# Performance work log

Hardware: AMD Instinct MI355X
Metric: run time of the kernel (lower is better)

The kernel has to match this reference:

```python
import jax, jax.numpy as jnp
import numpy as np
from jax import lax

D = 1024          # channel / embedding dim
K = 2048          # codebook size
BN_EPS = 1e-5


def conv1d(x, w, b, stride):
    # x: [N, C, L], w: [O, I, k]
    y = lax.conv_general_dilated(x, w, window_strides=(stride,), padding='VALID',
                                 dimension_numbers=('NCH', 'OIH', 'NCH'))
    return y + b[None, :, None]


def batchnorm1d(x, gamma, beta):
    # training-mode BN: batch statistics over (N, L) per channel, biased variance
    mean = jnp.mean(x, axis=(0, 2), keepdims=True)
    var = jnp.var(x, axis=(0, 2), keepdims=True)
    return (x - mean) * lax.rsqrt(var + BN_EPS) * gamma[None, :, None] + beta[None, :, None]


def setup_inputs() -> dict:
    key = jax.random.key(0)
    ks = jax.random.split(key, 8)
    x = jax.random.normal(ks[0], (32, D, 1024), dtype=jnp.float32)
    conv1_w = jax.random.normal(ks[1], (D, D, 4), dtype=jnp.float32) * 0.02
    conv1_b = jnp.zeros((D,), dtype=jnp.float32)
    bn1_g = jnp.ones((D,), dtype=jnp.float32)
    bn1_b = jnp.zeros((D,), dtype=jnp.float32)
    conv2_w = jax.random.normal(ks[2], (D, D, 1), dtype=jnp.float32) * 0.02
    conv2_b = jnp.zeros((D,), dtype=jnp.float32)
    bn2_g = jnp.ones((D,), dtype=jnp.float32)
    bn2_b = jnp.zeros((D,), dtype=jnp.float32)
    codebook = jax.random.normal(ks[3], (K, D), dtype=jnp.float32)
    return {'x': x, 'conv1_w': conv1_w, 'conv1_b': conv1_b,
            'bn1_g': bn1_g, 'bn1_b': bn1_b,
            'conv2_w': conv2_w, 'conv2_b': conv2_b,
            'bn2_g': bn2_g, 'bn2_b': bn2_b,
            'codebook': codebook}


def encoder(x, conv1_w, conv1_b, bn1_g, bn1_b, conv2_w, conv2_b, bn2_g, bn2_b):
    h = conv1d(x, conv1_w, conv1_b, stride=2)           # [B, D, L']
    # ResidualWrapper(BN -> ReLU -> Conv1x1)
    r = batchnorm1d(h, bn1_g, bn1_b)
    r = jax.nn.relu(r)
    r = conv1d(r, conv2_w, conv2_b, stride=1)
    h = h + r
    h = batchnorm1d(h, bn2_g, bn2_b)
    return h


def vq(h, codebook):
    # axis=1 -> move channel axis last: [B, L', D]
    z = jnp.moveaxis(h, 1, -1)
    # squared Euclidean distances via ||z||^2 - 2 z.e + ||e||^2  (cdist+argmin)
    z2 = jnp.sum(z * z, axis=-1, keepdims=True)                  # [B, L', 1]
    e2 = jnp.sum(codebook * codebook, axis=-1)                   # [K]
    ze = jnp.einsum('bld,kd->blk', z, codebook)                  # [B, L', K]
    dist2 = z2 - 2.0 * ze + e2[None, None, :]
    ids = jnp.argmin(dist2, axis=-1)                             # [B, L'] int
    q = codebook[ids]                                            # [B, L', D]
    sg = lax.stop_gradient
    commitment = jnp.mean((z - sg(q)) ** 2)
    codebook_loss = jnp.mean((sg(z) - q) ** 2)
    # straight-through estimator
    q_st = z + sg(q - z)
    q_st = jnp.moveaxis(q_st, -1, 1)                             # back to [B, D, L']
    return q_st, ids, commitment, codebook_loss


def reference(x, conv1_w, conv1_b, bn1_g, bn1_b, conv2_w, conv2_b, bn2_g, bn2_b, codebook):
    h = encoder(x, conv1_w, conv1_b, bn1_g, bn1_b, conv2_w, conv2_b, bn2_g, bn2_b)
    q_st, ids, commitment, codebook_loss = vq(h, codebook)
    return q_st, ids, commitment, codebook_loss
```

## Files before the change

### kernel.cpp

```cpp
#include <hip/hip_runtime.h>
#include <hip/hip_bf16.h>
#include <cstdint>

#define DD 1024
#define LIN 1024
#define LP 511
#define LPAD 512
#define NBATCH 32
#define KCB 2048
#define BN_EPS 1e-5f

#define OUT_IDS 16744448u
#define OUT_LOSS 16760800u

#define WS_H1 0
#define WS_UNI 16777216
#define WS_XH  (WS_UNI)
#define WS_XL  (WS_UNI + 16777728)
#define WS_WTH (WS_UNI + 33555456)
#define WS_WTL (WS_UNI + 35652608)
#define WS_T2  (WS_UNI)
#define WS_RH  (WS_UNI + 16777216)
#define WS_RL  (WS_UNI + 25165824)
#define WS_ZH  WS_RH
#define WS_ZL  WS_RL
#define WS_W2H (WS_UNI + 33554432)
#define WS_W2L (WS_UNI + 34078720)
#define WS_CBH (WS_UNI + 34603008)
#define WS_CBL (WS_UNI + 35651584)
#define WS_AUX (WS_UNI + 37749760)
#define WS_A1 (WS_AUX + 0)
#define WS_B1 (WS_AUX + 1024)
#define WS_A2 (WS_AUX + 2048)
#define WS_B2 (WS_AUX + 3072)
#define WS_E2 (WS_AUX + 4096)
#define WS_SLOTS (WS_AUX + 6144)
#define WS_LOSS (WS_AUX + 6144 + 32704)

typedef __attribute__((ext_vector_type(8))) short bf16x8;
typedef __attribute__((ext_vector_type(4))) float f32x4;
typedef __attribute__((ext_vector_type(16))) float f32x16;
typedef __attribute__((ext_vector_type(4))) unsigned short ushort4v;

__device__ __forceinline__ void async_cp16(const void* gsrc, void* ldst) {
  __builtin_amdgcn_global_load_lds(
      (const __attribute__((address_space(1))) unsigned int*)gsrc,
      (__attribute__((address_space(3))) unsigned int*)ldst, 16, 0, 0);
}

__device__ __forceinline__ void bf16split(float v, unsigned short& hi, unsigned short& lo) {
  __hip_bfloat16 h = __float2bfloat16(v);
  float hf = __bfloat162float(h);
  __hip_bfloat16 l = __float2bfloat16(v - hf);
  hi = *(unsigned short*)&h;
  lo = *(unsigned short*)&l;
}

__device__ inline float blockReduce256(float v, float* sb) {
#pragma unroll
  for (int off = 32; off > 0; off >>= 1) v += __shfl_down(v, off);
  __syncthreads();
  if ((threadIdx.x & 63) == 0) sb[threadIdx.x >> 6] = v;
  __syncthreads();
  return sb[0] + sb[1] + sb[2] + sb[3];
}

#define VMCNT(n) asm volatile("s_waitcnt vmcnt(" #n ")" ::: "memory")

template <typename SF>
__device__ __forceinline__ void stage_slot(const SF& sf, int c, int slot,
                                           unsigned short* smbase, int wid,
                                           int lane) {
  int plane, r0;
  if (slot < 4) {
    plane = 2 + (slot >> 1);
    r0 = ((slot & 1) << 7) + (wid << 4);
  } else {
    plane = wid & 1;
    r0 = (((wid >> 1) & 1) << 7) + ((slot - 4) << 5) + ((wid >> 2) << 4);
  }
  const unsigned short* g = sf(c, plane) + (size_t)(r0 + (lane >> 2)) * 1024 +
                            (((lane & 3) ^ ((lane >> 3) & 3)) << 3);
  unsigned short* d = smbase + plane * 8192 + r0 * 32;
  async_cp16(g, d);
}

template <typename SF>
__device__ __forceinline__ void mfma256_core32(const SF& sf, unsigned short* sm,
                                               int nkc, f32x16 (&acc)[4][2]) {
  const int tid = threadIdx.x;
  const int wid = tid >> 6, lane = tid & 63;
  const int wm = wid >> 2, wn = wid & 3;
  const int lrow = lane & 31;
  const int khalf = lane >> 5;
  const int sig = (lane >> 1) & 3;
  const int arowb = (wm << 7) + lrow;
  const int browb = (wn << 6) + lrow;

#pragma unroll
  for (int s = 0; s < 8; ++s) stage_slot(sf, 0, s, sm, wid, lane);

  bf16x8 fbh[2][2], fbl[2][2];
  for (int c = 0; c < nkc; ++c) {
    unsigned short* buf = sm + ((c & 1) << 15);
    unsigned short* nbuf = sm + (((c + 1) & 1) << 15);
    const unsigned short* As = buf;
    const unsigned short* Als = buf + 8192;
    const unsigned short* Bs = buf + 16384;
    const unsigned short* Bls = buf + 24576;
    const bool pre = (c + 1 < nkc);
#pragma unroll
    for (int q = 0; q < 2; ++q) {
      if (q == 0) {
        VMCNT(2);
      } else if (pre) {
        VMCNT(4);
      } else {
        VMCNT(0);
      }
      __builtin_amdgcn_s_barrier();
      asm volatile("" ::: "memory");
      __builtin_amdgcn_sched_barrier(0);
      if (q == 0) {
#pragma unroll
        for (int nt = 0; nt < 2; ++nt) {
          const int r = browb + nt * 32;
#pragma unroll
          for (int kh = 0; kh < 2; ++kh) {
            const int off = r * 32 + ((((kh << 1) + khalf) ^ sig) << 3);
            fbh[kh][nt] = *(const bf16x8*)(Bs + off);
            fbl[kh][nt] = *(const bf16x8*)(Bls + off);
          }
        }
      }
      bf16x8 fah[2][2], fal[2][2];
#pragma unroll
      for (int mi = 0; mi < 2; ++mi) {
        const int r = arowb + ((q << 1) + mi) * 32;
#pragma unroll
        for (int kh = 0; kh < 2; ++kh) {
          const int off = r * 32 + ((((kh << 1) + khalf) ^ sig) << 3);
          fah[mi][kh] = *(const bf16x8*)(As + off);
          fal[mi][kh] = *(const bf16x8*)(Als + off);
        }
      }
      if (pre) {
#pragma unroll
        for (int s = 0; s < 4; ++s)
          stage_slot(sf, c + 1, (q << 2) + s, nbuf, wid, lane);
      }
      __builtin_amdgcn_s_setprio(1);
#pragma unroll
      for (int kh = 0; kh < 2; ++kh) {
#pragma unroll
        for (int t = 0; t < 3; ++t) {
#pragma unroll
          for (int mi = 0; mi < 2; ++mi) {
#pragma unroll
            for (int nt = 0; nt < 2; ++nt) {
              const bf16x8 af = (t == 2) ? fal[mi][kh] : fah[mi][kh];
              const bf16x8 bb = (t == 1) ? fbl[kh][nt] : fbh[kh][nt];
              acc[(q << 1) + mi][nt] = __builtin_amdgcn_mfma_f32_32x32x16_bf16(
                  af, bb, acc[(q << 1) + mi][nt], 0, 0, 0);
            }
          }
        }
      }
      __builtin_amdgcn_s_setprio(0);
    }
  }
}

__global__ __launch_bounds__(256) void split_w1_kernel(
    const float* __restrict__ w, unsigned short* __restrict__ wth,
    unsigned short* __restrict__ wtl) {
  int idx = blockIdx.x * 256 + threadIdx.x;
  int o = idx >> 10, i = idx & 1023;
  float4 v = *(const float4*)&w[(size_t)idx * 4];
  float vv[4] = {v.x, v.y, v.z, v.w};
#pragma unroll
  for (int t = 0; t < 4; ++t) {
    unsigned short hi, lo;
    bf16split(vv[t], hi, lo);
    size_t off = (((size_t)(t << 10) + o) << 10) + i;
    wth[off] = hi;
    wtl[off] = lo;
  }
}

__global__ __launch_bounds__(256) void split_rows_kernel(
    const float* __restrict__ src, unsigned short* __restrict__ dsth,
    unsigned short* __restrict__ dstl) {
  size_t base = ((size_t)blockIdx.x * 256 + threadIdx.x) * 4;
  float4 v = *(const float4*)&src[base];
  float vv[4] = {v.x, v.y, v.z, v.w};
  ushort4v h, l;
#pragma unroll
  for (int j = 0; j < 4; ++j) {
    unsigned short hi, lo;
    bf16split(vv[j], hi, lo);
    h[j] = hi;
    l[j] = lo;
  }
  *(ushort4v*)&dsth[base] = h;
  *(ushort4v*)&dstl[base] = l;
}

__global__ __launch_bounds__(256) void split_x_kernel(
    const float* __restrict__ x, unsigned short* __restrict__ xh,
    unsigned short* __restrict__ xl) {
  __shared__ float lsT[128 * 65];
  const int l0 = blockIdx.x * 128;
  const int i0 = blockIdx.y * 64;
  const int nB = blockIdx.z;
  const int tid = threadIdx.x;
#pragma unroll
  for (int p = 0; p < 8; ++p) {
    int flat = p * 256 + tid;
    int row = flat >> 5, col4 = (flat & 31) * 4;
    float4 v = *(const float4*)&x[((size_t)nB * DD + i0 + row) * LIN + l0 + col4];
    lsT[(col4 + 0) * 65 + row] = v.x;
    lsT[(col4 + 1) * 65 + row] = v.y;
    lsT[(col4 + 2) * 65 + row] = v.z;
    lsT[(col4 + 3) * 65 + row] = v.w;
  }
  __syncthreads();
  const int lo2 = (l0 >> 1);
#pragma unroll
  for (int p = 0; p < 16; ++p) {
    int cp = p * 4 + (tid >> 6);
    int il = tid & 63;
    float vE = lsT[(2 * cp) * 65 + il];
    float vO = lsT[(2 * cp + 1) * 65 + il];
    unsigned short hE, lE, hO, lO;
    bf16split(vE, hE, lE);
    bf16split(vO, hO, lO);
    size_t dE = (((size_t)(0 * 32 + nB) * 512) + lo2 + cp) * 1024 + i0 + il;
    size_t dO = (((size_t)(1 * 32 + nB) * 512) + lo2 + cp) * 1024 + i0 + il;
    xh[dE] = hE; xl[dE] = lE;
    xh[dO] = hO; xl[dO] = lO;
  }
}

__global__ __launch_bounds__(256) void trans_affine_split_kernel(
    const float* __restrict__ src, const float* __restrict__ a,
    const float* __restrict__ b, unsigned short* __restrict__ dsth,
    unsigned short* __restrict__ dstl, int do_relu) {
  __shared__ float lsT[128 * 65];
  const int l0 = blockIdx.x * 128;
  const int i0 = blockIdx.y * 64;
  const int nB = blockIdx.z;
  const int tid = threadIdx.x;
#pragma unroll
  for (int p = 0; p < 8; ++p) {
    int flat = p * 256 + tid;
    int row = flat >> 5, col4 = (flat & 31) * 4;
    float4 v = *(const float4*)&src[((size_t)nB * DD + i0 + row) * LPAD + l0 + col4];
    lsT[(col4 + 0) * 65 + row] = v.x;
    lsT[(col4 + 1) * 65 + row] = v.y;
    lsT[(col4 + 2) * 65 + row] = v.z;
    lsT[(col4 + 3) * 65 + row] = v.w;
  }
  __syncthreads();
  const int il = tid & 63;
  const float ac = a[i0 + il], bc = b[i0 + il];
#pragma unroll
  for (int p = 0; p < 32; ++p) {
    int cp = p * 4 + (tid >> 6);
    float v = fmaf(ac, lsT[cp * 65 + il], bc);
    if (do_relu) v = fmaxf(v, 0.f);
    unsigned short hi, lo;
    bf16split(v, hi, lo);
    size_t d = (((size_t)nB * 512) + l0 + cp) * 1024 + i0 + il;
    dsth[d] = hi;
    dstl[d] = lo;
  }
}

__global__ __launch_bounds__(512, 2) void conv1_mfma_kernel(
    const unsigned short* __restrict__ wth, const unsigned short* __restrict__ wtl,
    const unsigned short* __restrict__ xh, const unsigned short* __restrict__ xl,
    const float* __restrict__ bias, float* __restrict__ h1) {
  extern __shared__ unsigned short sm[];
  const int tid = threadIdx.x;
  const int wid = tid >> 6, lane = tid & 63;
  const int lin = blockIdx.x;
  const int lb = (lin & 1) * 256;
  const int nB = ((lin >> 1) & 3) | ((lin >> 5) << 2);
  const int ob = ((lin >> 3) & 3) * 256;

  f32x16 acc[4][2];
#pragma unroll
  for (int a = 0; a < 4; ++a)
#pragma unroll
    for (int b = 0; b < 2; ++b)
#pragma unroll
      for (int e = 0; e < 16; ++e) acc[a][b][e] = 0.f;

  auto sf = [&](int c, int plane) -> const unsigned short* {
    int t = c >> 5, kc = c & 31;
    if (plane == 0) return wth + ((((size_t)t << 10) + ob) << 10) + kc * 32;
    if (plane == 1) return wtl + ((((size_t)t << 10) + ob) << 10) + kc * 32;
    const unsigned short* xp = (plane == 2) ? xh : xl;
    return xp + ((((size_t)((t & 1) * 32 + nB) * 512) + lb + (t >> 1)) << 10) + kc * 32;
  };
  mfma256_core32(sf, sm, 128, acc);

  const int wm = wid >> 2, wn = wid & 3;
#pragma unroll
  for (int mt = 0; mt < 4; ++mt) {
#pragma unroll
    for (int nt = 0; nt < 2; ++nt) {
      const int l = lb + (wn << 6) + nt * 32 + (lane & 31);
      if (l < LP) {
#pragma unroll
        for (int rq = 0; rq < 4; ++rq) {
          const int o0 = ob + (wm << 7) + mt * 32 + rq * 8 + ((lane >> 5) << 2);
#pragma unroll
          for (int rg = 0; rg < 4; ++rg)
            h1[((size_t)(nB << 10) + o0 + rg) * LPAD + l] =
                acc[mt][nt][rq * 4 + rg] + bias[o0 + rg];
        }
      }
    }
  }
}

__global__ __launch_bounds__(512, 2) void conv2_mfma_kernel(
    const unsigned short* __restrict__ w2h, const unsigned short* __restrict__ w2l,
    const unsigned short* __restrict__ rh, const unsigned short* __restrict__ rl,
    const float* __restrict__ b2c, const float* __restrict__ h1,
    float* __restrict__ t2) {
  extern __shared__ unsigned short sm[];
  const int tid = threadIdx.x;
  const int wid = tid >> 6, lane = tid & 63;
  const int lin = blockIdx.x;
  const int lb = (lin & 1) * 256;
  const int nB = ((lin >> 1) & 3) | ((lin >> 5) << 2);
  const int ob = ((lin >> 3) & 3) * 256;

  f32x16 acc[4][2];
#pragma unroll
  for (int a = 0; a < 4; ++a)
#pragma unroll
    for (int b = 0; b < 2; ++b)
#pragma unroll
      for (int e = 0; e < 16; ++e) acc[a][b][e] = 0.f;

  auto sf = [&](int c, int plane) -> const unsigned short* {
    if (plane == 0) return w2h + ((size_t)ob << 10) + (size_t)c * 32;
    if (plane == 1) return w2l + ((size_t)ob << 10) + (size_t)c * 32;
    const unsigned short* rp = (plane == 2) ? rh : rl;
    return rp + (((size_t)nB * 512 + lb) << 10) + (size_t)c * 32;
  };
  mfma256_core32(sf, sm, 32, acc);

  const int wm = wid >> 2, wn = wid & 3;
#pragma unroll
  for (int mt = 0; mt < 4; ++mt) {
#pragma unroll
    for (int nt = 0; nt < 2; ++nt) {
      const int l = lb + (wn << 6) + nt * 32 + (lane & 31);
      if (l < LP) {
#pragma unroll
        for (int rq = 0; rq < 4; ++rq) {
          const int o0 = ob + (wm << 7) + mt * 32 + rq * 8 + ((lane >> 5) << 2);
#pragma unroll
          for (int rg = 0; rg < 4; ++rg) {
            size_t off = ((size_t)(nB << 10) + o0 + rg) * LPAD + l;
            t2[off] = h1[off] + acc[mt][nt][rq * 4 + rg] + b2c[o0 + rg];
          }
        }
      }
    }
  }
}

__global__ __launch_bounds__(512, 2) void dist_mfma_kernel(
    const unsigned short* __restrict__ cbh, const unsigned short* __restrict__ cbl,
    const unsigned short* __restrict__ zh, const unsigned short* __restrict__ zl,
    const float* __restrict__ e2, unsigned long long* __restrict__ slots) {
  extern __shared__ unsigned short sm[];
  unsigned long long* best = (unsigned long long*)(sm + 65536);
  const int tid = threadIdx.x;
  const int wid = tid >> 6, lane = tid & 63;
  const int lb = blockIdx.x * 256, kb = blockIdx.y * 256, nB = blockIdx.z;

  if (tid < 256) best[tid] = ~0ULL;

  f32x16 acc[4][2];
#pragma unroll
  for (int a = 0; a < 4; ++a)
#pragma unroll
    for (int b = 0; b < 2; ++b)
#pragma unroll
      for (int e = 0; e < 16; ++e) acc[a][b][e] = 0.f;

  auto sf = [&](int c, int plane) -> const unsigned short* {
    if (plane == 0) return cbh + ((size_t)kb << 10) + (size_t)c * 32;
    if (plane == 1) return cbl + ((size_t)kb << 10) + (size_t)c * 32;
    const unsigned short* zp = (plane == 2) ? zh : zl;
    return zp + (((size_t)nB * 512 + lb) << 10) + (size_t)c * 32;
  };
  mfma256_core32(sf, sm, 32, acc);

  const int wm = wid >> 2, wn = wid & 3;
#pragma unroll
  for (int nt = 0; nt < 2; ++nt) {
    const int col = (wn << 6) + nt * 32 + (lane & 31);
    float dmin = 3.4e38f;
    int kmin = 0;
#pragma unroll
    for (int mt = 0; mt < 4; ++mt) {
#pragma unroll
      for (int rq = 0; rq < 4; ++rq) {
        const int kbase = kb + (wm << 7) + mt * 32 + rq * 8 + ((lane >> 5) << 2);
#pragma unroll
        for (int rg = 0; rg < 4; ++rg) {
          float dist = fmaf(-2.f, acc[mt][nt][rq * 4 + rg], e2[kbase + rg]);
          if (dist < dmin) { dmin = dist; kmin = kbase + rg; }
        }
      }
    }
    unsigned long long pk =
        ((unsigned long long)__float_as_uint(dmin) << 32) | (unsigned)kmin;
    atomicMin(&best[col], pk);
  }
  __syncthreads();
  if (tid < 256) {
    int l = lb + tid;
    if (l < LP) atomicMin(&slots[(size_t)nB * LP + l], best[tid]);
  }
}

__global__ __launch_bounds__(256) void bn_stats_kernel(
    const float* __restrict__ src, const float* __restrict__ gamma,
    const float* __restrict__ beta, float* __restrict__ a_out,
    float* __restrict__ b_out) {
  __shared__ float sb[4];
  const int c = blockIdx.x;
  const float* p = src + (size_t)c * LPAD;
  float s1 = 0.f, s2 = 0.f;
  for (int idx = threadIdx.x; idx < NBATCH * LP; idx += 256) {
    int nn = idx / LP;
    int l = idx - nn * LP;
    float v = p[(size_t)nn * DD * LPAD + l];
    s1 += v;
    s2 = fmaf(v, v, s2);
  }
  s1 = blockReduce256(s1, sb);
  s2 = blockReduce256(s2, sb);
  if (threadIdx.x == 0) {
    const float inv = 1.f / (float)(NBATCH * LP);
    float m = s1 * inv;
    float var = fmaf(-m, m, s2 * inv);
    float a = gamma[c] * rsqrtf(var + BN_EPS);
    a_out[c] = a;
    b_out[c] = fmaf(-m, a, beta[c]);
  }
}

__global__ __launch_bounds__(256) void e2_kernel(const float* __restrict__ cb,
                                                 float* __restrict__ e2) {
  __shared__ float sb[4];
  const int k = blockIdx.x;
  float s = 0.f;
  for (int d = threadIdx.x; d < DD; d += 256) {
    float v = cb[(size_t)k * DD + d];
    s = fmaf(v, v, s);
  }
  s = blockReduce256(s, sb);
  if (threadIdx.x == 0) e2[k] = s;
}

__global__ __launch_bounds__(256) void gather_kernel(
    const float* __restrict__ t2, const float* __restrict__ cb,
    const float* __restrict__ a2, const float* __restrict__ b2,
    const unsigned long long* __restrict__ slots, float* __restrict__ out,
    float* __restrict__ loss_acc) {
  __shared__ int ks[64];
  __shared__ float sb[4];
  const int l0 = blockIdx.x * 64;
  const int n = blockIdx.y;
  const int tid = threadIdx.x, tx = tid & 63, ty = tid >> 6;
  if (tid < 64) {
    int l = l0 + tid;
    int k = 0;
    if (l < LP) {
      k = (int)(unsigned)(slots[(size_t)n * LP + l] & 0xffffffffULL);
      out[OUT_IDS + (size_t)n * LP + l] = (float)k;
    }
    ks[tid] = k;
  }
  __syncthreads();
  const int l = l0 + tx;
  const bool valid = (l < LP);
  const int k = ks[tx];
  const float* cbk = cb + (size_t)k * DD;
  const float* tn = t2 + (size_t)n * DD * LPAD;
  float* qo = out + (size_t)n * DD * LP;
  float lsum = 0.f;
  for (int d0 = 0; d0 < DD; d0 += 4) {
    const int d = d0 + ty;
    float q = cbk[d];
    if (valid) {
      float z = fmaf(a2[d], tn[(size_t)d * LPAD + l], b2[d]);
      qo[(size_t)d * LP + l] = q;
      float e = z - q;
      lsum = fmaf(e, e, lsum);
    }
  }
  lsum = blockReduce256(lsum, sb);
  if (tid == 0) atomicAdd(loss_acc, lsum);
}

__global__ void finalize_kernel(const float* __restrict__ loss_acc,
                                float* __restrict__ out) {
  if (threadIdx.x == 0) {
    float m = loss_acc[0] * (1.f / 16744448.f);
    out[OUT_LOSS] = m;
    out[OUT_LOSS + 1] = m;
  }
}

extern "C" void kernel_launch(void* const* d_in, const int* in_sizes, int n_in,
                              void* d_out, int out_size, void* d_ws,
                              size_t ws_size, hipStream_t stream) {
  const float* x = (const float*)d_in[0];
  const float* w1 = (const float*)d_in[1];
  const float* b1c = (const float*)d_in[2];
  const float* g1 = (const float*)d_in[3];
  const float* be1 = (const float*)d_in[4];
  const float* w2 = (const float*)d_in[5];
  const float* b2c = (const float*)d_in[6];
  const float* g2 = (const float*)d_in[7];
  const float* be2 = (const float*)d_in[8];
  const float* cb = (const float*)d_in[9];
  float* out = (float*)d_out;
  float* ws = (float*)d_ws;

  float* h1 = ws + WS_H1;
  float* t2 = ws + WS_T2;
  unsigned short* xh = (unsigned short*)(ws + WS_XH);
  unsigned short* xl = (unsigned short*)(ws + WS_XL);
  unsigned short* wth = (unsigned short*)(ws + WS_WTH);
  unsigned short* wtl = (unsigned short*)(ws + WS_WTL);
  unsigned short* rh = (unsigned short*)(ws + WS_RH);
  unsigned short* rl = (unsigned short*)(ws + WS_RL);
  unsigned short* zh = (unsigned short*)(ws + WS_ZH);
  unsigned short* zl = (unsigned short*)(ws + WS_ZL);
  unsigned short* w2h = (unsigned short*)(ws + WS_W2H);
  unsigned short* w2l = (unsigned short*)(ws + WS_W2L);
  unsigned short* cbh = (unsigned short*)(ws + WS_CBH);
  unsigned short* cbl = (unsigned short*)(ws + WS_CBL);
  float* a1 = ws + WS_A1;
  float* bb1 = ws + WS_B1;
  float* a2 = ws + WS_A2;
  float* bb2 = ws + WS_B2;
  float* e2 = ws + WS_E2;
  unsigned long long* slots = (unsigned long long*)(ws + WS_SLOTS);
  float* loss = ws + WS_LOSS;

  static int attr_done = 0;
  if (!attr_done) {
    (void)hipFuncSetAttribute(reinterpret_cast<const void*>(conv1_mfma_kernel),
                              hipFuncAttributeMaxDynamicSharedMemorySize, 135168);
    (void)hipFuncSetAttribute(reinterpret_cast<const void*>(conv2_mfma_kernel),
                              hipFuncAttributeMaxDynamicSharedMemorySize, 135168);
    (void)hipFuncSetAttribute(reinterpret_cast<const void*>(dist_mfma_kernel),
                              hipFuncAttributeMaxDynamicSharedMemorySize, 135168);
    attr_done = 1;
  }

  (void)hipMemsetAsync(slots, 0xFF,
                       (size_t)NBATCH * LP * sizeof(unsigned long long), stream);
  (void)hipMemsetAsync(loss, 0, sizeof(float), stream);

  split_w1_kernel<<<4096, 256, 0, stream>>>(w1, wth, wtl);
  split_x_kernel<<<dim3(8, 16, NBATCH), 256, 0, stream>>>(x, xh, xl);
  conv1_mfma_kernel<<<256, 512, 131072, stream>>>(wth, wtl, xh, xl, b1c, h1);
  bn_stats_kernel<<<DD, 256, 0, stream>>>(h1, g1, be1, a1, bb1);
  split_rows_kernel<<<1024, 256, 0, stream>>>(w2, w2h, w2l);
  split_rows_kernel<<<2048, 256, 0, stream>>>(cb, cbh, cbl);
  e2_kernel<<<KCB, 256, 0, stream>>>(cb, e2);
  trans_affine_split_kernel<<<dim3(4, 16, NBATCH), 256, 0, stream>>>(
      h1, a1, bb1, rh, rl, 1);
  conv2_mfma_kernel<<<256, 512, 131072, stream>>>(w2h, w2l, rh, rl, b2c, h1, t2);
  bn_stats_kernel<<<DD, 256, 0, stream>>>(t2, g2, be2, a2, bb2);
  trans_affine_split_kernel<<<dim3(4, 16, NBATCH), 256, 0, stream>>>(
      t2, a2, bb2, zh, zl, 0);
  dist_mfma_kernel<<<dim3(2, 8, NBATCH), 512, 133120, stream>>>(cbh, cbl, zh,
                                                                zl, e2, slots);
  gather_kernel<<<dim3(8, NBATCH), 256, 0, stream>>>(t2, cb, a2, bb2, slots, out, loss);
  finalize_kernel<<<1, 64, 0, stream>>>(loss, out);
}
```

Measured before the change: 1.025 ms.

## Software-pipeline MFMA GEMM core with register prefetch of next-chunk LDS fragments

Rewrites the bf16x3 MFMA main loop as a manually unrolled two-chunk pipeline. Fragments for the next k-chunk are read from LDS into registers while the current chunk's MFMAs run, and global-to-LDS staging is issued two chunks ahead in split halves. The aim is to hide LDS read latency and barrier stalls behind matrix instructions. The cost is higher register pressure and more complex wait-count logic, and the loop now assumes an even chunk count of at least 2.

```diff
diff --git a/kernel.cpp b/kernel.cpp
--- a/kernel.cpp
+++ b/kernel.cpp
@@ -85,6 +85,101 @@
   async_cp16(g, d);
 }
 
+template <int PH>
+__device__ __forceinline__ void mfma_half(f32x16 (&acc)[4][2],
+                                          const bf16x8 (&ah)[2],
+                                          const bf16x8 (&al)[2],
+                                          const bf16x8 (&bh)[2],
+                                          const bf16x8 (&bl)[2]) {
+#pragma unroll
+  for (int t = 0; t < 3; ++t)
+#pragma unroll
+    for (int mi = 0; mi < 2; ++mi)
+#pragma unroll
+      for (int nt = 0; nt < 2; ++nt) {
+        const bf16x8 af = (t == 2) ? al[mi] : ah[mi];
+        const bf16x8 bb = (t == 1) ? bl[nt] : bh[nt];
+        acc[PH * 2 + mi][nt] = __builtin_amdgcn_mfma_f32_32x32x16_bf16(
+            af, bb, acc[PH * 2 + mi][nt], 0, 0, 0);
+      }
+}
+
+#define FRAG(BASE, ROW, SIDX) \
+  (*(const bf16x8*)((BASE) + (ROW) * 32 + (((SIDX) ^ sig) << 3)))
+
+#define CHUNK_BODY(CIDX, PP, NX1, NX2)                                        \
+  {                                                                           \
+    const int c__ = (CIDX);                                                   \
+    unsigned short* bufc = sm + ((PP) << 15);                                 \
+    unsigned short* bufn = sm + (((PP) ^ 1) << 15);                           \
+    const unsigned short* As = bufc;                                          \
+    const unsigned short* Als = bufc + 8192;                                  \
+    const unsigned short* Bs = bufc + 16384;                                  \
+    const unsigned short* Bls = bufc + 24576;                                 \
+    const unsigned short* Asn = bufn;                                         \
+    const unsigned short* Alsn = bufn + 8192;                                 \
+    const unsigned short* Bsn = bufn + 16384;                                 \
+    const unsigned short* Blsn = bufn + 24576;                                \
+                                                            \
+    if (NX1) { VMCNT(4); } else { VMCNT(0); }                                 \
+    __builtin_amdgcn_s_barrier();                                             \
+    __builtin_amdgcn_sched_barrier(0);                                        \
+    _Pragma("unroll") for (int mi = 0; mi < 2; ++mi) {                        \
+      const int r = arowb + mi * 32;                                          \
+      a0h[1][mi] = FRAG(As, r, 2 + khalf);                                    \
+      a0l[1][mi] = FRAG(Als, r, 2 + khalf);                                   \
+    }                                                                         \
+    _Pragma("unroll") for (int nt = 0; nt < 2; ++nt) {                        \
+      const int r = browb + nt * 32;                                          \
+      bh1[nt] = FRAG(Bs, r, 2 + khalf);                                       \
+      bl1[nt] = FRAG(Bls, r, 2 + khalf);                                      \
+    }                                                                         \
+    _Pragma("unroll") for (int mi = 0; mi < 2; ++mi) {                        \
+      const int r = arowb + (2 + mi) * 32;                                    \
+      a1h[0][mi] = FRAG(As, r, khalf);                                        \
+      a1l[0][mi] = FRAG(Als, r, khalf);                                       \
+    }                                                                         \
+    if (NX1) {                                                                \
+      _Pragma("unroll") for (int s = 4; s < 8; ++s)                           \
+          stage_slot(sf, c__ + 1, s, bufn, wid, lane);                        \
+    }                                                                         \
+    __builtin_amdgcn_sched_barrier(0);                                        \
+    __builtin_amdgcn_s_setprio(1);                                            \
+    mfma_half<0>(acc, a0h[0], a0l[0], bh0[PP], bl0[PP]);                      \
+    mfma_half<0>(acc, a0h[1], a0l[1], bh1, bl1);                              \
+    __builtin_amdgcn_s_setprio(0);                                            \
+                                                            \
+    if (NX1) { VMCNT(2); } else { VMCNT(0); }                                 \
+    __builtin_amdgcn_s_barrier();                                             \
+    __builtin_amdgcn_sched_barrier(0);                                        \
+    _Pragma("unroll") for (int mi = 0; mi < 2; ++mi) {                        \
+      const int r = arowb + (2 + mi) * 32;                                    \
+      a1h[1][mi] = FRAG(As, r, 2 + khalf);                                    \
+      a1l[1][mi] = FRAG(Als, r, 2 + khalf);                                   \
+    }                                                                         \
+    if (NX1) {                                                                \
+      _Pragma("unroll") for (int nt = 0; nt < 2; ++nt) {                      \
+        const int r = browb + nt * 32;                                        \
+        bh0[(PP) ^ 1][nt] = FRAG(Bsn, r, khalf);                              \
+        bl0[(PP) ^ 1][nt] = FRAG(Blsn, r, khalf);                             \
+      }                                                                       \
+      _Pragma("unroll") for (int mi = 0; mi < 2; ++mi) {                      \
+        const int r = arowb + mi * 32;                                        \
+        a0h[0][mi] = FRAG(Asn, r, khalf);                                     \
+        a0l[0][mi] = FRAG(Alsn, r, khalf);                                    \
+      }                                                                       \
+    }                                                                         \
+    if (NX2) {                                                                \
+      _Pragma("unroll") for (int s = 0; s < 4; ++s)                           \
+          stage_slot(sf, c__ + 2, s, bufc, wid, lane);                        \
+    }                                                                         \
+    __builtin_amdgcn_sched_barrier(0);                                        \
+    __builtin_amdgcn_s_setprio(1);                                            \
+    mfma_half<1>(acc, a1h[0], a1l[0], bh0[PP], bl0[PP]);                      \
+    mfma_half<1>(acc, a1h[1], a1l[1], bh1, bl1);                              \
+    __builtin_amdgcn_s_setprio(0);                                            \
+  }
+
 template <typename SF>
 __device__ __forceinline__ void mfma256_core32(const SF& sf, unsigned short* sm,
                                                int nkc, f32x16 (&acc)[4][2]) {
@@ -97,78 +192,43 @@
   const int arowb = (wm << 7) + lrow;
   const int browb = (wn << 6) + lrow;
 
+  bf16x8 a0h[2][2], a0l[2][2];
+  bf16x8 a1h[2][2], a1l[2][2];
+  bf16x8 bh0[2][2], bl0[2][2];
+  bf16x8 bh1[2], bl1[2];
+
 #pragma unroll
   for (int s = 0; s < 8; ++s) stage_slot(sf, 0, s, sm, wid, lane);
-
-  bf16x8 fbh[2][2], fbl[2][2];
-  for (int c = 0; c < nkc; ++c) {
-    unsigned short* buf = sm + ((c & 1) << 15);
-    unsigned short* nbuf = sm + (((c + 1) & 1) << 15);
-    const unsigned short* As = buf;
-    const unsigned short* Als = buf + 8192;
-    const unsigned short* Bs = buf + 16384;
-    const unsigned short* Bls = buf + 24576;
-    const bool pre = (c + 1 < nkc);
-#pragma unroll
-    for (int q = 0; q < 2; ++q) {
-      if (q == 0) {
-        VMCNT(2);
-      } else if (pre) {
-        VMCNT(4);
-      } else {
-        VMCNT(0);
-      }
-      __builtin_amdgcn_s_barrier();
-      asm volatile("" ::: "memory");
-      __builtin_amdgcn_sched_barrier(0);
-      if (q == 0) {
-#pragma unroll
-        for (int nt = 0; nt < 2; ++nt) {
-          const int r = browb + nt * 32;
-#pragma unroll
-          for (int kh = 0; kh < 2; ++kh) {
-            const int off = r * 32 + ((((kh << 1) + khalf) ^ sig) << 3);
-            fbh[kh][nt] = *(const bf16x8*)(Bs + off);
-            fbl[kh][nt] = *(const bf16x8*)(Bls + off);
-          }
-        }
-      }
-      bf16x8 fah[2][2], fal[2][2];
-#pragma unroll
-      for (int mi = 0; mi < 2; ++mi) {
-        const int r = arowb + ((q << 1) + mi) * 32;
-#pragma unroll
-        for (int kh = 0; kh < 2; ++kh) {
-          const int off = r * 32 + ((((kh << 1) + khalf) ^ sig) << 3);
-          fah[mi][kh] = *(const bf16x8*)(As + off);
-          fal[mi][kh] = *(const bf16x8*)(Als + off);
-        }
-      }
-      if (pre) {
-#pragma unroll
-        for (int s = 0; s < 4; ++s)
-          stage_slot(sf, c + 1, (q << 2) + s, nbuf, wid, lane);
-      }
-      __builtin_amdgcn_s_setprio(1);
-#pragma unroll
-      for (int kh = 0; kh < 2; ++kh) {
-#pragma unroll
-        for (int t = 0; t < 3; ++t) {
-#pragma unroll
-          for (int mi = 0; mi < 2; ++mi) {
-#pragma unroll
-            for (int nt = 0; nt < 2; ++nt) {
-              const bf16x8 af = (t == 2) ? fal[mi][kh] : fah[mi][kh];
-              const bf16x8 bb = (t == 1) ? fbl[kh][nt] : fbh[kh][nt];
-              acc[(q << 1) + mi][nt] = __builtin_amdgcn_mfma_f32_32x32x16_bf16(
-                  af, bb, acc[(q << 1) + mi][nt], 0, 0, 0);
-            }
-          }
-        }
-      }
-      __builtin_amdgcn_s_setprio(0);
+#pragma unroll
+  for (int s = 0; s < 4; ++s) stage_slot(sf, 1, s, sm + 32768, wid, lane);
+  VMCNT(4);
+  __builtin_amdgcn_s_barrier();
+  __builtin_amdgcn_sched_barrier(0);
+  {
+    const unsigned short* As = sm;
+    const unsigned short* Als = sm + 8192;
+    const unsigned short* Bs = sm + 16384;
+    const unsigned short* Bls = sm + 24576;
+#pragma unroll
+    for (int nt = 0; nt < 2; ++nt) {
+      const int r = browb + nt * 32;
+      bh0[0][nt] = FRAG(Bs, r, khalf);
+      bl0[0][nt] = FRAG(Bls, r, khalf);
     }
-  }
+#pragma unroll
+    for (int mi = 0; mi < 2; ++mi) {
+      const int r = arowb + mi * 32;
+      a0h[0][mi] = FRAG(As, r, khalf);
+      a0l[0][mi] = FRAG(Als, r, khalf);
+    }
+  }
+
+  for (int cc = 0; cc < nkc - 2; cc += 2) {
+    CHUNK_BODY(cc, 0, true, true);
+    CHUNK_BODY(cc + 1, 1, true, true);
+  }
+  CHUNK_BODY(nkc - 2, 0, true, false);
+  CHUNK_BODY(nkc - 1, 1, false, false);
 }
 
 __global__ __launch_bounds__(256) void split_w1_kernel(
```

Result: slower. 1.486 ms (+45.0%).
